# Performance work log

Hardware: AMD Instinct MI355X
Metric: run time of the kernel (lower is better)

## Reference

```python
import jax, jax.numpy as jnp
import numpy as np

E = 8        # num_experts
TOP_K = 2
D = 1024     # embeddings_dims
H = 2 * D    # swiglu hidden dims


def setup_inputs() -> dict:
    key = jax.random.key(0)
    k0, k1, k2, k3, k4 = jax.random.split(key, 5)
    scale = 0.02
    x = jax.random.normal(k0, (4, 2048, D), dtype=jnp.float32)
    Wg = jax.random.normal(k1, (D, E), dtype=jnp.float32) * scale   # router gate
    W1 = jax.random.normal(k2, (E, D, H), dtype=jnp.float32) * scale  # linear_layer1 per expert
    W2 = jax.random.normal(k3, (E, D, H), dtype=jnp.float32) * scale  # linear_layer2 per expert
    W3 = jax.random.normal(k4, (E, H, D), dtype=jnp.float32) * scale  # linear_layer3 per expert
    return {"x": x, "Wg": Wg, "W1": W1, "W2": W2, "W3": W3}


def reference(x, Wg, W1, W2, W3):
    # Router: gate -> top-k -> softmax over the k selected logits
    logits = jnp.einsum('bsd,de->bse', x, Wg)              # [B,S,E]
    top_vals, top_idx = jax.lax.top_k(logits, TOP_K)       # [B,S,K]
    probs = jax.nn.softmax(top_vals, axis=-1)              # [B,S,K]
    # Per-expert combine weight: sum of probs where the expert was selected
    onehot = jax.nn.one_hot(top_idx, E, dtype=x.dtype)     # [B,S,K,E]
    weights = jnp.einsum('bsk,bske->bse', probs, onehot)   # [B,S,E]

    out = jnp.zeros_like(x)
    for e in range(E):  # fixed small structural loop over experts
        u = jnp.einsum('bsd,dh->bsh', x, W1[e])
        v = jnp.einsum('bsd,dh->bsh', x, W2[e])
        h = (u * jax.nn.sigmoid(u)) * v                    # SwiGLU: swish(u) * v
        y = jnp.einsum('bsh,hd->bsd', h, W3[e])
        out = out + y * weights[..., e][..., None]
    return out
```

## Files before the change

### kernel.cpp

```cpp
#include <hip/hip_runtime.h>
#include <stdint.h>

#define T_TOKENS 8192
#define D_DIM 1024
#define H_DIM 2048
#define E_NUM 8
#define MAXP 18432
#define MAXT 72
#define NCHUNK 32

typedef __attribute__((ext_vector_type(8))) short short8;
typedef __attribute__((ext_vector_type(4))) float f32x4;
typedef __attribute__((ext_vector_type(8))) unsigned short u16x8;

__device__ __forceinline__ unsigned short f2bf(float f) {
  union { float f; uint32_t u; } v; v.f = f;
  uint32_t r = (v.u + 0x7fffu + ((v.u >> 16) & 1u)) >> 16;
  return (unsigned short)r;
}

__device__ __forceinline__ float bf2f(unsigned short u) {
  union { uint32_t u; float f; } v; v.u = ((uint32_t)u) << 16;
  return v.f;
}

__device__ __forceinline__ void gload16(const void* g, void* l) {
  __builtin_amdgcn_global_load_lds((const __attribute__((address_space(1))) void*)g,
                                   (__attribute__((address_space(3))) void*)l, 16, 0, 0);
}

__global__ void router_kernel(const float* __restrict__ x, const float* __restrict__ Wg,
                              int* __restrict__ tok_e01, float* __restrict__ tok_w) {
  __shared__ float wgT[E_NUM * D_DIM];
  int tid = threadIdx.x;
  for (int i = tid; i < D_DIM * E_NUM; i += 256) {
    int e = i >> 10, d = i & 1023;
    wgT[e * D_DIM + d] = Wg[d * E_NUM + e];
  }
  __syncthreads();
  int wid = tid >> 6, lane = tid & 63;
  int t = blockIdx.x * 4 + wid;
  const float* xr = x + (size_t)t * D_DIM;
  double acc[E_NUM];
#pragma unroll
  for (int e = 0; e < E_NUM; e++) acc[e] = 0.0;
  for (int i = 0; i < D_DIM / 64; i++) {
    double xv = (double)xr[i * 64 + lane];
#pragma unroll
    for (int e = 0; e < E_NUM; e++) acc[e] += xv * (double)wgT[e * D_DIM + i * 64 + lane];
  }
#pragma unroll
  for (int e = 0; e < E_NUM; e++) {
    double v = acc[e];
#pragma unroll
    for (int off = 32; off >= 1; off >>= 1) v += __shfl_xor(v, off);
    acc[e] = v;
  }
  if (lane == 0) {
    int e0 = 0; double l0 = acc[0];
#pragma unroll
    for (int e = 1; e < E_NUM; e++) if (acc[e] > l0) { l0 = acc[e]; e0 = e; }
    int e1 = -1; double l1 = -1e300;
#pragma unroll
    for (int e = 0; e < E_NUM; e++) if (e != e0 && acc[e] > l1) { l1 = acc[e]; e1 = e; }
    float z1 = expf((float)(l1 - l0));
    float w0 = 1.f / (1.f + z1);
    float w1 = z1 * w0;
    tok_e01[t] = e0 | (e1 << 8);
    tok_w[2 * t] = w0; tok_w[2 * t + 1] = w1;
  }
}

__global__ void hist_kernel(const int* __restrict__ tok_e01, int* __restrict__ poffs,
                            int* __restrict__ tile2e, int* __restrict__ tile_row0,
                            int* __restrict__ chunk_base) {
  __shared__ int chist[NCHUNK][E_NUM];
  int tid = threadIdx.x, wv = tid >> 6, lane = tid & 63;
#pragma unroll
  for (int half = 0; half < 2; half++) {
    int myc = 0;
#pragma unroll
    for (int it = 0; it < 4; it++) {
      int t = wv * 512 + half * 256 + it * 64 + lane;
      int p = tok_e01[t];
      int e0 = p & 255, e1 = (p >> 8) & 255;
#pragma unroll
      for (int e = 0; e < E_NUM; e++) {
        unsigned long long b0 = __ballot(e0 == e);
        unsigned long long b1 = __ballot(e1 == e);
        if (lane == e) myc += __popcll(b0) + __popcll(b1);
      }
    }
    if (lane < E_NUM) chist[wv * 2 + half][lane] = myc;
  }
  __syncthreads();
  if (tid == 0) {
    int tot[E_NUM];
    for (int e = 0; e < E_NUM; e++) {
      int s = 0;
      for (int c = 0; c < NCHUNK; c++) s += chist[c][e];
      tot[e] = s;
    }
    int po = 0, tf = 0;
    for (int e = 0; e < E_NUM; e++) {
      poffs[e] = po;
      int nt = (tot[e] + 255) >> 8;
      for (int i = 0; i < nt; i++) { tile2e[tf] = e; tile_row0[tf] = po + i * 256; tf++; }
      po += nt << 8;
    }
    for (; tf < MAXT; tf++) { tile2e[tf] = -1; tile_row0[tf] = 0; }
    for (int e = 0; e < E_NUM; e++) {
      int s = poffs[e];
      for (int c = 0; c < NCHUNK; c++) { chunk_base[c * E_NUM + e] = s; s += chist[c][e]; }
    }
  }
}

__global__ void assign_kernel(const int* __restrict__ tok_e01, const int* __restrict__ chunk_base,
                              int* __restrict__ pair_tok, int2* __restrict__ tok_pos) {
  __shared__ int wcnt[4][E_NUM];
  __shared__ int woff[4][E_NUM];
  int tid = threadIdx.x, wv = tid >> 6, lane = tid & 63;
  int t = blockIdx.x * 256 + tid;
  int p = tok_e01[t];
  int e0 = p & 255, e1 = (p >> 8) & 255;
  unsigned long long lt = (lane == 63) ? ~0ull >> 1 : (1ull << lane) - 1;
  int rank0 = 0, rank1 = 0, myc = 0;
#pragma unroll
  for (int e = 0; e < E_NUM; e++) {
    unsigned long long b0 = __ballot(e0 == e);
    unsigned long long b1 = __ballot(e1 == e);
    int n0 = __popcll(b0);
    if (e0 == e) rank0 = __popcll(b0 & lt);
    if (e1 == e) rank1 = n0 + __popcll(b1 & lt);
    if (lane == e) myc = n0 + __popcll(b1);
  }
  if (lane < E_NUM) wcnt[wv][lane] = myc;
  __syncthreads();
  if (tid < E_NUM) {
    int s = 0;
    for (int w = 0; w < 4; w++) { woff[w][tid] = s; s += wcnt[w][tid]; }
  }
  __syncthreads();
  int cb = blockIdx.x * E_NUM;
  int pos0 = chunk_base[cb + e0] + woff[wv][e0] + rank0;
  int pos1 = chunk_base[cb + e1] + woff[wv][e1] + rank1;
  pair_tok[pos0] = t;
  pair_tok[pos1] = t;
  tok_pos[t] = make_int2(pos0, pos1);
}

__global__ void cast_x_kernel(const float* __restrict__ x, unsigned short* __restrict__ xb) {
  int i = blockIdx.x * 256 + threadIdx.x;
  const float4* xp = (const float4*)x;
  float4 a = xp[2 * i], b = xp[2 * i + 1];
  u16x8 r;
  r[0] = f2bf(a.x); r[1] = f2bf(a.y); r[2] = f2bf(a.z); r[3] = f2bf(a.w);
  r[4] = f2bf(b.x); r[5] = f2bf(b.y); r[6] = f2bf(b.z); r[7] = f2bf(b.w);
  *(u16x8*)(xb + (size_t)i * 8) = r;
}

__global__ void cast_transpose_kernel(const float* __restrict__ in, unsigned short* __restrict__ out,
                                      int R, int C) {
  __shared__ float tile[32][33];
  int e = blockIdx.z;
  const float* src = in + (size_t)e * R * C;
  unsigned short* dst = out + (size_t)e * R * C;
  int c0 = blockIdx.x * 32, r0 = blockIdx.y * 32;
  int tx = threadIdx.x, ty = threadIdx.y;
#pragma unroll
  for (int i = 0; i < 4; i++)
    tile[ty + i * 8][tx] = src[(size_t)(r0 + ty + i * 8) * C + c0 + tx];
  __syncthreads();
#pragma unroll
  for (int i = 0; i < 4; i++)
    dst[(size_t)(c0 + ty + i * 8) * R + r0 + tx] = f2bf(tile[tx][ty + i * 8]);
}

__global__ void cast_transpose_cat_kernel(const float* __restrict__ in, unsigned short* __restrict__ Bcat,
                                          int isV) {
  __shared__ float tile[32][33];
  int e = blockIdx.z;
  const float* src = in + (size_t)e * D_DIM * H_DIM;
  unsigned short* dst = Bcat + (size_t)e * 4096 * 1024;
  int c0 = blockIdx.x * 32, r0 = blockIdx.y * 32;
  int tx = threadIdx.x, ty = threadIdx.y;
#pragma unroll
  for (int i = 0; i < 4; i++)
    tile[ty + i * 8][tx] = src[(size_t)(r0 + ty + i * 8) * H_DIM + c0 + tx];
  __syncthreads();
#pragma unroll
  for (int i = 0; i < 4; i++) {
    int n = c0 + ty + i * 8;
    int nr = ((n >> 4) << 5) + (n & 15) + isV * 16;
    dst[(size_t)nr * 1024 + r0 + tx] = f2bf(tile[tx][ty + i * 8]);
  }
}

__global__ __launch_bounds__(512, 2) void ffn1_kernel(
    const unsigned short* __restrict__ xb, const unsigned short* __restrict__ Bcat,
    unsigned short* __restrict__ h_buf,
    const int* __restrict__ pair_tok, const int* __restrict__ tile2e,
    const int* __restrict__ tile_row0) {
  extern __shared__ char lds[];
  char* ldsB = lds + 65536;
  const int NWG = MAXT * 16;
  int orig = blockIdx.x;
  int wg = (orig & 7) * (NWG >> 3) + (orig >> 3);
  int f = wg >> 4, nt = wg & 15;
  int e = tile2e[f];
  if (e < 0) return;
  int row0 = tile_row0[f];

  int tid = threadIdx.x;
  int w = tid >> 6, lane = tid & 63;
  int l15 = lane & 15, g4 = lane >> 4;
  int wr = w >> 2, wn = w & 3;

  int s0 = w * 64 + lane;
  int r0_ = s0 >> 3, c0_ = s0 & 7;
  int kc = c0_ ^ (r0_ & 7);
  const char* gA[2][2];
  const char* gB[2][2];
  const char* Bce = (const char*)Bcat + (size_t)e * 4096 * 2048;
#pragma unroll
  for (int h = 0; h < 2; h++) {
    int tokA0 = pair_tok[row0 + h * 128 + r0_];
    int tokA1 = pair_tok[row0 + h * 128 + r0_ + 64];
    gA[h][0] = (const char*)xb + (size_t)tokA0 * 2048 + kc * 16;
    gA[h][1] = (const char*)xb + (size_t)tokA1 * 2048 + kc * 16;
    gB[h][0] = Bce + (size_t)(nt * 256 + h * 128 + r0_) * 2048 + kc * 16;
    gB[h][1] = Bce + (size_t)(nt * 256 + h * 128 + r0_ + 64) * 2048 + kc * 16;
  }

  auto STG_A = [&](int kt, int h, int buf) {
    char* d = lds + buf * 32768 + h * 16384 + w * 1024;
    gload16(gA[h][0] + kt * 128, d);
    gload16(gA[h][1] + kt * 128, d + 8192);
  };
  auto STG_B = [&](int kt, int h, int buf) {
    char* d = ldsB + buf * 32768 + h * 16384 + w * 1024;
    gload16(gB[h][0] + kt * 128, d);
    gload16(gB[h][1] + kt * 128, d + 8192);
  };

  int sw = l15 & 7;
  int cbase = (sw >> 2) * 64 + ((g4 ^ (sw & 3)) * 16);
  int aRow = wr * 16384 + l15 * 128;
  int bRow = 65536 + wn * 8192 + l15 * 128;

  f32x4 acc[8][4];
#pragma unroll
  for (int i = 0; i < 8; i++)
#pragma unroll
    for (int j = 0; j < 4; j++) acc[i][j] = (f32x4){0.f, 0.f, 0.f, 0.f};

  short8 a[4][2], blo[2][2], bhi[2][2];
  auto RD_A = [&](int mq, int buf) {
    const char* base = lds + buf * 32768 + aRow + mq * 8192;
#pragma unroll
    for (int m2 = 0; m2 < 4; m2++)
#pragma unroll
      for (int ks = 0; ks < 2; ks++)
        a[m2][ks] = *(const short8*)(base + m2 * 2048 + (cbase ^ (ks << 6)));
  };
  auto RD_B = [&](short8 (&b)[2][2], int nq, int buf) {
    const char* base = lds + buf * 32768 + bRow + nq * 4096;
#pragma unroll
    for (int n2 = 0; n2 < 2; n2++)
#pragma unroll
      for (int ks = 0; ks < 2; ks++)
        b[n2][ks] = *(const short8*)(base + n2 * 2048 + (cbase ^ (ks << 6)));
  };
  auto MM = [&](int mq, short8 (&b)[2][2], int nq) {
    __builtin_amdgcn_s_setprio(1);
#pragma unroll
    for (int m2 = 0; m2 < 4; m2++)
#pragma unroll
      for (int n2 = 0; n2 < 2; n2++)
#pragma unroll
        for (int ks = 0; ks < 2; ks++)
          acc[mq * 4 + m2][nq * 2 + n2] = __builtin_amdgcn_mfma_f32_16x16x32_bf16(
              a[m2][ks], b[n2][ks], acc[mq * 4 + m2][nq * 2 + n2], 0, 0, 0);
    __builtin_amdgcn_s_setprio(0);
  };

  STG_A(0, 0, 0); STG_A(0, 1, 0); STG_B(0, 0, 0); STG_B(0, 1, 0);
  STG_B(1, 0, 1); STG_A(1, 0, 1);
  asm volatile("s_waitcnt vmcnt(4)" ::: "memory");
  __builtin_amdgcn_s_barrier();
  asm volatile("" ::: "memory");

  const int NT = 16;
#pragma unroll 1
  for (int kt = 0; kt < NT; kt++) {
    int buf = kt & 1;
    RD_A(0, buf); RD_B(blo, 0, buf);
    if (kt + 1 < NT) STG_A(kt + 1, 1, buf ^ 1);
    __builtin_amdgcn_s_barrier();
    asm volatile("" ::: "memory");
    MM(0, blo, 0);
    __builtin_amdgcn_s_barrier();
    asm volatile("" ::: "memory");
    RD_B(bhi, 1, buf);
    if (kt + 1 < NT) STG_B(kt + 1, 1, buf ^ 1);
    __builtin_amdgcn_s_barrier();
    asm volatile("" ::: "memory");
    MM(0, bhi, 1);
    __builtin_amdgcn_s_barrier();
    asm volatile("" ::: "memory");
    RD_A(1, buf);
    if (kt + 2 < NT) STG_B(kt + 2, 0, buf);
    __builtin_amdgcn_s_barrier();
    asm volatile("" ::: "memory");
    MM(1, bhi, 1);
    __builtin_amdgcn_s_barrier();
    asm volatile("" ::: "memory");
    if (kt + 2 < NT) STG_A(kt + 2, 0, buf);
    if (kt < NT - 2) {
      asm volatile("s_waitcnt vmcnt(4)" ::: "memory");
    } else if (kt == NT - 2) {
      asm volatile("s_waitcnt vmcnt(0)" ::: "memory");
    }
    __builtin_amdgcn_s_barrier();
    asm volatile("" ::: "memory");
    MM(1, blo, 0);
    __builtin_amdgcn_s_barrier();
    asm volatile("" ::: "memory");
  }

#pragma unroll
  for (int mf = 0; mf < 8; mf++) {
#pragma unroll
    for (int p = 0; p < 2; p++) {
      f32x4 uu = acc[mf][2 * p], vv = acc[mf][2 * p + 1];
      int hcol = (nt * 8 + wn * 2 + p) * 16 + l15;
#pragma unroll
      for (int rr = 0; rr < 4; rr++) {
        int r_out = row0 + wr * 128 + mf * 16 + g4 * 4 + rr;
        float xx = uu[rr];
        float hh = (xx / (1.f + __expf(-xx))) * vv[rr];
        h_buf[(size_t)r_out * H_DIM + hcol] = f2bf(hh);
      }
    }
  }
}

__global__ __launch_bounds__(256, 3) void ffn2_kernel(
    const unsigned short* __restrict__ h_buf, const unsigned short* __restrict__ W3t,
    unsigned short* __restrict__ y_buf,
    const int* __restrict__ tile2e, const int* __restrict__ tile_row0) {
  const int NWG = MAXT * 8;
  int orig = blockIdx.x;
  int wg = (orig & 7) * (NWG >> 3) + (orig >> 3);
  int f = wg >> 3, nt = wg & 7;
  int e = tile2e[f];
  if (e < 0) return;
  int row0 = tile_row0[f] + blockIdx.y * 128;

  __shared__ alignas(16) char ldsA[2][8192];
  __shared__ alignas(16) char ldsB[2][8192];

  int tid = threadIdx.x, w = tid >> 6, lane = tid & 63;
  int l15 = lane & 15, g4 = lane >> 4;
  int wr = w >> 1, wc = w & 1;

  int r = tid >> 2;
  int qs = (tid & 3) ^ ((r >> 1) & 3);
  const char* gA0 = (const char*)h_buf + (size_t)(row0 + r) * 4096 + qs * 16;
  const char* gA1 = (const char*)h_buf + (size_t)(row0 + r + 64) * 4096 + qs * 16;
  const char* W3e = (const char*)W3t + (size_t)e * 1024 * 4096;
  const char* gB0 = W3e + (size_t)(nt * 128 + r) * 4096 + qs * 16;
  const char* gB1 = W3e + (size_t)(nt * 128 + r + 64) * 4096 + qs * 16;

  auto STG = [&](int buf, int ks) {
    int ko = ks * 64;
    char* dA = &ldsA[buf][w * 1024];
    char* dB = &ldsB[buf][w * 1024];
    gload16(gA0 + ko, dA); gload16(gA1 + ko, dA + 4096);
    gload16(gB0 + ko, dB); gload16(gB1 + ko, dB + 4096);
  };

  int qr = g4 ^ ((l15 >> 1) & 3);
  int aoff[4], boff[4];
#pragma unroll
  for (int i = 0; i < 4; i++) {
    aoff[i] = (wr * 64 + i * 16 + l15) * 64 + qr * 16;
    boff[i] = (wc * 64 + i * 16 + l15) * 64 + qr * 16;
  }

  f32x4 acc[4][4];
#pragma unroll
  for (int i = 0; i < 4; i++)
#pragma unroll
    for (int j = 0; j < 4; j++) acc[i][j] = (f32x4){0.f, 0.f, 0.f, 0.f};

  const int NK = 64;
  STG(0, 0);
  __syncthreads();
#pragma unroll 1
  for (int ks = 0; ks < NK; ks++) {
    int cur = ks & 1;
    if (ks + 1 < NK) STG(cur ^ 1, ks + 1);
    short8 af[4], bf[4];
#pragma unroll
    for (int i = 0; i < 4; i++) {
      af[i] = *(const short8*)(&ldsA[cur][aoff[i]]);
      bf[i] = *(const short8*)(&ldsB[cur][boff[i]]);
    }
#pragma unroll
    for (int i = 0; i < 4; i++)
#pragma unroll
      for (int j = 0; j < 4; j++)
        acc[i][j] = __builtin_amdgcn_mfma_f32_16x16x32_bf16(af[i], bf[j], acc[i][j], 0, 0, 0);
    if (ks + 1 < NK) __syncthreads();
  }

#pragma unroll
  for (int mf = 0; mf < 4; mf++) {
#pragma unroll
    for (int nf = 0; nf < 4; nf++) {
      int col = nt * 128 + wc * 64 + nf * 16 + l15;
#pragma unroll
      for (int rr = 0; rr < 4; rr++) {
        int pos = row0 + wr * 64 + mf * 16 + g4 * 4 + rr;
        y_buf[(size_t)pos * D_DIM + col] = f2bf(acc[mf][nf][rr]);
      }
    }
  }
}

__global__ void combine_kernel(const unsigned short* __restrict__ y_buf,
                               const int2* __restrict__ tok_pos, const float* __restrict__ tok_w,
                               float* __restrict__ out) {
  int t = blockIdx.x * 2 + (threadIdx.x >> 7);
  int c = (threadIdx.x & 127) * 8;
  int2 p = tok_pos[t];
  float w0 = tok_w[2 * t], w1 = tok_w[2 * t + 1];
  u16x8 a = *(const u16x8*)(y_buf + (size_t)p.x * D_DIM + c);
  u16x8 b = *(const u16x8*)(y_buf + (size_t)p.y * D_DIM + c);
  float o[8];
#pragma unroll
  for (int k = 0; k < 8; k++) o[k] = w0 * bf2f(a[k]) + w1 * bf2f(b[k]);
  float4* op = (float4*)(out + (size_t)t * D_DIM + c);
  op[0] = make_float4(o[0], o[1], o[2], o[3]);
  op[1] = make_float4(o[4], o[5], o[6], o[7]);
}

extern "C" void kernel_launch(void* const* d_in, const int* in_sizes, int n_in,
                              void* d_out, int out_size, void* d_ws, size_t ws_size,
                              hipStream_t stream) {
  const float* x  = (const float*)d_in[0];
  const float* Wg = (const float*)d_in[1];
  const float* W1 = (const float*)d_in[2];
  const float* W2 = (const float*)d_in[3];
  const float* W3 = (const float*)d_in[4];
  float* out = (float*)d_out;

  char* ws = (char*)d_ws;
  size_t off = 0;
  auto alloc = [&](size_t bytes) -> char* {
    char* p = ws + off; off += (bytes + 255) & ~(size_t)255; return p;
  };

  int*            poffs      = (int*)alloc(16 * 4);
  int*            tile2e     = (int*)alloc(80 * 4);
  int*            tile_row0  = (int*)alloc(80 * 4);
  int*            chunk_base = (int*)alloc(NCHUNK * E_NUM * 4);
  int*            tok_e01    = (int*)alloc(T_TOKENS * 4);
  float*          tok_w      = (float*)alloc(T_TOKENS * 8);
  int2*           tok_pos    = (int2*)alloc(T_TOKENS * 8);
  int*            pair_tok   = (int*)alloc(MAXP * 4);
  unsigned short* xb         = (unsigned short*)alloc((size_t)T_TOKENS * D_DIM * 2);
  unsigned short* Bcat       = (unsigned short*)alloc((size_t)E_NUM * 4096 * 1024 * 2);
  unsigned short* W3t        = (unsigned short*)alloc((size_t)E_NUM * D_DIM * H_DIM * 2);
  unsigned short* h_buf      = (unsigned short*)alloc((size_t)MAXP * H_DIM * 2);
  unsigned short* y_buf      = Bcat;

  hipFuncSetAttribute((const void*)ffn1_kernel, hipFuncAttributeMaxDynamicSharedMemorySize, 131072);

  hipMemsetAsync(pair_tok, 0, MAXP * 4, stream);

  router_kernel<<<T_TOKENS / 4, 256, 0, stream>>>(x, Wg, tok_e01, tok_w);
  hist_kernel<<<1, 1024, 0, stream>>>(tok_e01, poffs, tile2e, tile_row0, chunk_base);
  assign_kernel<<<NCHUNK, 256, 0, stream>>>(tok_e01, chunk_base, pair_tok, tok_pos);
  cast_x_kernel<<<(T_TOKENS * D_DIM / 8) / 256, 256, 0, stream>>>(x, xb);
  dim3 tb(32, 8);
  cast_transpose_cat_kernel<<<dim3(H_DIM / 32, D_DIM / 32, E_NUM), tb, 0, stream>>>(W1, Bcat, 0);
  cast_transpose_cat_kernel<<<dim3(H_DIM / 32, D_DIM / 32, E_NUM), tb, 0, stream>>>(W2, Bcat, 1);
  cast_transpose_kernel<<<dim3(D_DIM / 32, H_DIM / 32, E_NUM), tb, 0, stream>>>(W3, W3t, H_DIM, D_DIM);

  ffn1_kernel<<<dim3(MAXT * 16), 512, 131072, stream>>>(xb, Bcat, h_buf, pair_tok, tile2e, tile_row0);
  ffn2_kernel<<<dim3(MAXT * 8, 2), 256, 0, stream>>>(h_buf, W3t, y_buf, tile2e, tile_row0);
  combine_kernel<<<T_TOKENS / 2, 256, 0, stream>>>(y_buf, tok_pos, tok_w, out);
}
```

Baseline: 431.7 us.

## Rework ffn2 as 256x256 eight-wave pipelined GEMM and vectorize weight cast-transposes

The ffn2 GEMM moves from 128x128 tiles with 4 waves and simple double buffering to 256x256 tiles with 8 waves and 128 KB of dynamic LDS. It uses a split-phase schedule that interleaves half-tile global loads, LDS reads and MFMA blocks between barriers, with XOR-swizzled LDS and raised wave priority during MFMAs. The three weight cast-transpose kernels are merged into one 64x64-tile kernel with float4 loads and 16-byte bf16 stores. The larger tile cuts global traffic per FLOP, but yields fewer workgroups and relies on careful vmcnt bookkeeping.

```diff
diff --git a/kernel.cpp b/kernel.cpp
--- a/kernel.cpp
+++ b/kernel.cpp
@@ -160,41 +160,32 @@
   *(u16x8*)(xb + (size_t)i * 8) = r;
 }
 
-__global__ void cast_transpose_kernel(const float* __restrict__ in, unsigned short* __restrict__ out,
-                                      int R, int C) {
-  __shared__ float tile[32][33];
+__global__ void cast_transpose64_kernel(const float* __restrict__ in, unsigned short* __restrict__ out,
+                                        int R, int C, size_t e_stride, int cat, int voff) {
+  __shared__ float tile[64][68];
   int e = blockIdx.z;
   const float* src = in + (size_t)e * R * C;
-  unsigned short* dst = out + (size_t)e * R * C;
-  int c0 = blockIdx.x * 32, r0 = blockIdx.y * 32;
-  int tx = threadIdx.x, ty = threadIdx.y;
-#pragma unroll
-  for (int i = 0; i < 4; i++)
-    tile[ty + i * 8][tx] = src[(size_t)(r0 + ty + i * 8) * C + c0 + tx];
+  unsigned short* dst = out + (size_t)e * e_stride;
+  int c0 = blockIdx.x * 64, r0 = blockIdx.y * 64;
+  int tl = threadIdx.x;
+  int lr = tl >> 4, lc = (tl & 15) * 4;
+#pragma unroll
+  for (int p = 0; p < 4; p++) {
+    float4 v = *(const float4*)(src + (size_t)(r0 + p * 16 + lr) * C + c0 + lc);
+    *(float4*)&tile[p * 16 + lr][lc] = v;
+  }
   __syncthreads();
-#pragma unroll
-  for (int i = 0; i < 4; i++)
-    dst[(size_t)(c0 + ty + i * 8) * R + r0 + tx] = f2bf(tile[tx][ty + i * 8]);
-}
-
-__global__ void cast_transpose_cat_kernel(const float* __restrict__ in, unsigned short* __restrict__ Bcat,
-                                          int isV) {
-  __shared__ float tile[32][33];
-  int e = blockIdx.z;
-  const float* src = in + (size_t)e * D_DIM * H_DIM;
-  unsigned short* dst = Bcat + (size_t)e * 4096 * 1024;
-  int c0 = blockIdx.x * 32, r0 = blockIdx.y * 32;
-  int tx = threadIdx.x, ty = threadIdx.y;
-#pragma unroll
-  for (int i = 0; i < 4; i++)
-    tile[ty + i * 8][tx] = src[(size_t)(r0 + ty + i * 8) * H_DIM + c0 + tx];
-  __syncthreads();
-#pragma unroll
-  for (int i = 0; i < 4; i++) {
-    int n = c0 + ty + i * 8;
-    int nr = ((n >> 4) << 5) + (n & 15) + isV * 16;
-    dst[(size_t)nr * 1024 + r0 + tx] = f2bf(tile[tx][ty + i * 8]);
-  }
+  int cc = tl >> 2, rchunk = (tl & 3) * 16;
+  int n = c0 + cc;
+  int outrow = cat ? (((n >> 4) << 5) + (n & 15) + voff * 16) : n;
+  u16x8 o0, o1;
+#pragma unroll
+  for (int k = 0; k < 8; k++) o0[k] = f2bf(tile[rchunk + k][cc]);
+#pragma unroll
+  for (int k = 0; k < 8; k++) o1[k] = f2bf(tile[rchunk + 8 + k][cc]);
+  unsigned short* dp = dst + (size_t)outrow * R + r0 + rchunk;
+  *(u16x8*)dp = o0;
+  *(u16x8*)(dp + 8) = o1;
 }
 
 __global__ __launch_bounds__(512, 2) void ffn1_kernel(
@@ -346,84 +337,143 @@
   }
 }
 
-__global__ __launch_bounds__(256, 3) void ffn2_kernel(
+__global__ __launch_bounds__(512, 2) void ffn2_kernel(
     const unsigned short* __restrict__ h_buf, const unsigned short* __restrict__ W3t,
     unsigned short* __restrict__ y_buf,
     const int* __restrict__ tile2e, const int* __restrict__ tile_row0) {
-  const int NWG = MAXT * 8;
+  extern __shared__ char lds[];
+  char* ldsB = lds + 65536;
+  const int NWG = MAXT * 4;
   int orig = blockIdx.x;
   int wg = (orig & 7) * (NWG >> 3) + (orig >> 3);
-  int f = wg >> 3, nt = wg & 7;
+  int f = wg >> 2, nt = wg & 3;
   int e = tile2e[f];
   if (e < 0) return;
-  int row0 = tile_row0[f] + blockIdx.y * 128;
-
-  __shared__ alignas(16) char ldsA[2][8192];
-  __shared__ alignas(16) char ldsB[2][8192];
-
-  int tid = threadIdx.x, w = tid >> 6, lane = tid & 63;
+  int row0 = tile_row0[f];
+
+  int tid = threadIdx.x;
+  int w = tid >> 6, lane = tid & 63;
   int l15 = lane & 15, g4 = lane >> 4;
-  int wr = w >> 1, wc = w & 1;
-
-  int r = tid >> 2;
-  int qs = (tid & 3) ^ ((r >> 1) & 3);
-  const char* gA0 = (const char*)h_buf + (size_t)(row0 + r) * 4096 + qs * 16;
-  const char* gA1 = (const char*)h_buf + (size_t)(row0 + r + 64) * 4096 + qs * 16;
+  int wr = w >> 2, wn = w & 3;
+
+  int s0 = w * 64 + lane;
+  int r0_ = s0 >> 3, c0_ = s0 & 7;
+  int kc = c0_ ^ (r0_ & 7);
+  const char* gA[2][2];
+  const char* gB[2][2];
   const char* W3e = (const char*)W3t + (size_t)e * 1024 * 4096;
-  const char* gB0 = W3e + (size_t)(nt * 128 + r) * 4096 + qs * 16;
-  const char* gB1 = W3e + (size_t)(nt * 128 + r + 64) * 4096 + qs * 16;
-
-  auto STG = [&](int buf, int ks) {
-    int ko = ks * 64;
-    char* dA = &ldsA[buf][w * 1024];
-    char* dB = &ldsB[buf][w * 1024];
-    gload16(gA0 + ko, dA); gload16(gA1 + ko, dA + 4096);
-    gload16(gB0 + ko, dB); gload16(gB1 + ko, dB + 4096);
-  };
-
-  int qr = g4 ^ ((l15 >> 1) & 3);
-  int aoff[4], boff[4];
-#pragma unroll
-  for (int i = 0; i < 4; i++) {
-    aoff[i] = (wr * 64 + i * 16 + l15) * 64 + qr * 16;
-    boff[i] = (wc * 64 + i * 16 + l15) * 64 + qr * 16;
-  }
-
-  f32x4 acc[4][4];
-#pragma unroll
-  for (int i = 0; i < 4; i++)
+#pragma unroll
+  for (int h = 0; h < 2; h++) {
+    gA[h][0] = (const char*)h_buf + (size_t)(row0 + h * 128 + r0_) * 4096 + kc * 16;
+    gA[h][1] = (const char*)h_buf + (size_t)(row0 + h * 128 + r0_ + 64) * 4096 + kc * 16;
+    gB[h][0] = W3e + (size_t)(nt * 256 + h * 128 + r0_) * 4096 + kc * 16;
+    gB[h][1] = W3e + (size_t)(nt * 256 + h * 128 + r0_ + 64) * 4096 + kc * 16;
+  }
+
+  auto STG_A = [&](int kt, int h, int buf) {
+    char* d = lds + buf * 32768 + h * 16384 + w * 1024;
+    gload16(gA[h][0] + kt * 128, d);
+    gload16(gA[h][1] + kt * 128, d + 8192);
+  };
+  auto STG_B = [&](int kt, int h, int buf) {
+    char* d = ldsB + buf * 32768 + h * 16384 + w * 1024;
+    gload16(gB[h][0] + kt * 128, d);
+    gload16(gB[h][1] + kt * 128, d + 8192);
+  };
+
+  int sw = l15 & 7;
+  int cbase = (sw >> 2) * 64 + ((g4 ^ (sw & 3)) * 16);
+  int aRow = wr * 16384 + l15 * 128;
+  int bRow = 65536 + wn * 8192 + l15 * 128;
+
+  f32x4 acc[8][4];
+#pragma unroll
+  for (int i = 0; i < 8; i++)
 #pragma unroll
     for (int j = 0; j < 4; j++) acc[i][j] = (f32x4){0.f, 0.f, 0.f, 0.f};
 
-  const int NK = 64;
-  STG(0, 0);
-  __syncthreads();
+  short8 a[4][2], blo[2][2], bhi[2][2];
+  auto RD_A = [&](int mq, int buf) {
+    const char* base = lds + buf * 32768 + aRow + mq * 8192;
+#pragma unroll
+    for (int m2 = 0; m2 < 4; m2++)
+#pragma unroll
+      for (int ks = 0; ks < 2; ks++)
+        a[m2][ks] = *(const short8*)(base + m2 * 2048 + (cbase ^ (ks << 6)));
+  };
+  auto RD_B = [&](short8 (&b)[2][2], int nq, int buf) {
+    const char* base = lds + buf * 32768 + bRow + nq * 4096;
+#pragma unroll
+    for (int n2 = 0; n2 < 2; n2++)
+#pragma unroll
+      for (int ks = 0; ks < 2; ks++)
+        b[n2][ks] = *(const short8*)(base + n2 * 2048 + (cbase ^ (ks << 6)));
+  };
+  auto MM = [&](int mq, short8 (&b)[2][2], int nq) {
+    __builtin_amdgcn_s_setprio(1);
+#pragma unroll
+    for (int m2 = 0; m2 < 4; m2++)
+#pragma unroll
+      for (int n2 = 0; n2 < 2; n2++)
+#pragma unroll
+        for (int ks = 0; ks < 2; ks++)
+          acc[mq * 4 + m2][nq * 2 + n2] = __builtin_amdgcn_mfma_f32_16x16x32_bf16(
+              a[m2][ks], b[n2][ks], acc[mq * 4 + m2][nq * 2 + n2], 0, 0, 0);
+    __builtin_amdgcn_s_setprio(0);
+  };
+
+  STG_A(0, 0, 0); STG_A(0, 1, 0); STG_B(0, 0, 0); STG_B(0, 1, 0);
+  STG_B(1, 0, 1); STG_A(1, 0, 1);
+  asm volatile("s_waitcnt vmcnt(4)" ::: "memory");
+  __builtin_amdgcn_s_barrier();
+  asm volatile("" ::: "memory");
+
+  const int NT = 32;
 #pragma unroll 1
-  for (int ks = 0; ks < NK; ks++) {
-    int cur = ks & 1;
-    if (ks + 1 < NK) STG(cur ^ 1, ks + 1);
-    short8 af[4], bf[4];
-#pragma unroll
-    for (int i = 0; i < 4; i++) {
-      af[i] = *(const short8*)(&ldsA[cur][aoff[i]]);
-      bf[i] = *(const short8*)(&ldsB[cur][boff[i]]);
-    }
-#pragma unroll
-    for (int i = 0; i < 4; i++)
-#pragma unroll
-      for (int j = 0; j < 4; j++)
-        acc[i][j] = __builtin_amdgcn_mfma_f32_16x16x32_bf16(af[i], bf[j], acc[i][j], 0, 0, 0);
-    if (ks + 1 < NK) __syncthreads();
-  }
-
-#pragma unroll
-  for (int mf = 0; mf < 4; mf++) {
+  for (int kt = 0; kt < NT; kt++) {
+    int buf = kt & 1;
+    RD_A(0, buf); RD_B(blo, 0, buf);
+    if (kt + 1 < NT) STG_A(kt + 1, 1, buf ^ 1);
+    __builtin_amdgcn_s_barrier();
+    asm volatile("" ::: "memory");
+    MM(0, blo, 0);
+    __builtin_amdgcn_s_barrier();
+    asm volatile("" ::: "memory");
+    RD_B(bhi, 1, buf);
+    if (kt + 1 < NT) STG_B(kt + 1, 1, buf ^ 1);
+    __builtin_amdgcn_s_barrier();
+    asm volatile("" ::: "memory");
+    MM(0, bhi, 1);
+    __builtin_amdgcn_s_barrier();
+    asm volatile("" ::: "memory");
+    RD_A(1, buf);
+    if (kt + 2 < NT) STG_B(kt + 2, 0, buf);
+    __builtin_amdgcn_s_barrier();
+    asm volatile("" ::: "memory");
+    MM(1, bhi, 1);
+    __builtin_amdgcn_s_barrier();
+    asm volatile("" ::: "memory");
+    if (kt + 2 < NT) STG_A(kt + 2, 0, buf);
+    if (kt < NT - 2) {
+      asm volatile("s_waitcnt vmcnt(4)" ::: "memory");
+    } else if (kt == NT - 2) {
+      asm volatile("s_waitcnt vmcnt(0)" ::: "memory");
+    }
+    __builtin_amdgcn_s_barrier();
+    asm volatile("" ::: "memory");
+    MM(1, blo, 0);
+    __builtin_amdgcn_s_barrier();
+    asm volatile("" ::: "memory");
+  }
+
+#pragma unroll
+  for (int mf = 0; mf < 8; mf++) {
 #pragma unroll
     for (int nf = 0; nf < 4; nf++) {
-      int col = nt * 128 + wc * 64 + nf * 16 + l15;
+      int col = nt * 256 + wn * 64 + nf * 16 + l15;
 #pragma unroll
       for (int rr = 0; rr < 4; rr++) {
-        int pos = row0 + wr * 64 + mf * 16 + g4 * 4 + rr;
+        int pos = row0 + wr * 128 + mf * 16 + g4 * 4 + rr;
         y_buf[(size_t)pos * D_DIM + col] = f2bf(acc[mf][nf][rr]);
       }
     }
@@ -478,6 +528,7 @@
   unsigned short* y_buf      = Bcat;
 
   hipFuncSetAttribute((const void*)ffn1_kernel, hipFuncAttributeMaxDynamicSharedMemorySize, 131072);
+  hipFuncSetAttribute((const void*)ffn2_kernel, hipFuncAttributeMaxDynamicSharedMemorySize, 131072);
 
   hipMemsetAsync(pair_tok, 0, MAXP * 4, stream);
 
@@ -485,12 +536,14 @@
   hist_kernel<<<1, 1024, 0, stream>>>(tok_e01, poffs, tile2e, tile_row0, chunk_base);
   assign_kernel<<<NCHUNK, 256, 0, stream>>>(tok_e01, chunk_base, pair_tok, tok_pos);
   cast_x_kernel<<<(T_TOKENS * D_DIM / 8) / 256, 256, 0, stream>>>(x, xb);
-  dim3 tb(32, 8);
-  cast_transpose_cat_kernel<<<dim3(H_DIM / 32, D_DIM / 32, E_NUM), tb, 0, stream>>>(W1, Bcat, 0);
-  cast_transpose_cat_kernel<<<dim3(H_DIM / 32, D_DIM / 32, E_NUM), tb, 0, stream>>>(W2, Bcat, 1);
-  cast_transpose_kernel<<<dim3(D_DIM / 32, H_DIM / 32, E_NUM), tb, 0, stream>>>(W3, W3t, H_DIM, D_DIM);
+  cast_transpose64_kernel<<<dim3(H_DIM / 64, D_DIM / 64, E_NUM), 256, 0, stream>>>(
+      W1, Bcat, D_DIM, H_DIM, (size_t)4096 * 1024, 1, 0);
+  cast_transpose64_kernel<<<dim3(H_DIM / 64, D_DIM / 64, E_NUM), 256, 0, stream>>>(
+      W2, Bcat, D_DIM, H_DIM, (size_t)4096 * 1024, 1, 1);
+  cast_transpose64_kernel<<<dim3(D_DIM / 64, H_DIM / 64, E_NUM), 256, 0, stream>>>(
+      W3, W3t, H_DIM, D_DIM, (size_t)2048 * 1024, 0, 0);
 
   ffn1_kernel<<<dim3(MAXT * 16), 512, 131072, stream>>>(xb, Bcat, h_buf, pair_tok, tile2e, tile_row0);
-  ffn2_kernel<<<dim3(MAXT * 8, 2), 256, 0, stream>>>(h_buf, W3t, y_buf, tile2e, tile_row0);
+  ffn2_kernel<<<dim3(MAXT * 4), 512, 131072, stream>>>(h_buf, W3t, y_buf, tile2e, tile_row0);
   combine_kernel<<<T_TOKENS / 2, 256, 0, stream>>>(y_buf, tok_pos, tok_w, out);
 }
```

Result: no change. 429.6 us (-0.5%).
